# Performance work log

Hardware: AMD Instinct MI355X
Metric: run time of the kernel (lower is better)

The kernel has to match this reference:

```python
import jax, jax.numpy as jnp
import numpy as np

N_NODES = 100000
N_EDGES = 3200000
IN_DIM = 256
EMB_DIM = 64
BATCH = 4096
WEIGHT_DECAY = 1e-4


def setup_inputs() -> dict:
    key = jax.random.key(0)
    ks = jax.random.split(key, 8)
    feats = jax.random.normal(ks[0], (N_NODES, IN_DIM), dtype=jnp.float32)
    W = jax.random.normal(ks[1], (IN_DIM, EMB_DIM), dtype=jnp.float32) * (1.0 / np.sqrt(IN_DIM))
    edge_row = jax.random.randint(ks[2], (N_EDGES,), 0, N_NODES, dtype=jnp.int32)
    edge_col = jax.random.randint(ks[3], (N_EDGES,), 0, N_NODES, dtype=jnp.int32)
    edge_val = jax.random.uniform(ks[4], (N_EDGES,), dtype=jnp.float32) * 0.05  # normalized adj weights
    idx1 = jax.random.randint(ks[5], (BATCH,), 0, N_NODES, dtype=jnp.int32)
    idx2 = jax.random.randint(ks[6], (BATCH,), 0, N_NODES, dtype=jnp.int32)
    neg_idx = jax.random.randint(ks[7], (BATCH,), 0, N_NODES, dtype=jnp.int32)
    return {"feats": feats, "W": W, "edge_row": edge_row, "edge_col": edge_col,
            "edge_val": edge_val, "idx1": idx1, "idx2": idx2, "neg_idx": neg_idx}


def reference(feats, W, edge_row, edge_col, edge_val, idx1, idx2, neg_idx):
    # GraphConvolution: tanh( A_sparse @ (X @ W) ), A in COO form
    xw = feats @ W                                              # [N, D]
    msgs = edge_val[:, None] * xw[edge_col]                     # [E, D] gather + scale
    h = jax.ops.segment_sum(msgs, edge_row, num_segments=N_NODES)  # sparse-dense matmul
    h = jnp.tanh(h)
    # tf.nn.l2_normalize(embedding, 1)
    sq = jnp.sum(h * h, axis=1, keepdims=True)
    emb = h * jax.lax.rsqrt(jnp.maximum(sq, 1e-12))             # [N, D]
    # embedding lookups
    o1, o2, on = emb[idx1], emb[idx2], emb[neg_idx]             # [B, D] each
    y_ui = jnp.sum(o1 * o2, axis=1)
    y_uj = jnp.sum(o1 * on, axis=1)
    # BPR loss + weight decay (tf.nn.l2_loss = 0.5*sum(x^2))
    bpr = jnp.sum(-jax.nn.log_sigmoid(y_ui - y_uj))
    loss = (bpr + WEIGHT_DECAY * 0.5 * jnp.sum(emb * emb)) / jnp.float32(BATCH)
    return loss
```

## Files before the change

### kernel.cpp

```cpp
#include <hip/hip_runtime.h>
#include <cmath>

#define N_NODES 100000
#define N_EDGES 3200000
#define IN_DIM 256
#define EMB 64
#define BATCH 4096
#define MWAVES 6250
#define NBUCK 782
#define BROWS 128
#define BSTRIDE 4608
#define PSTRIDE 5504
#define EPB 4096

typedef unsigned long long u64;
typedef unsigned int u32;
typedef unsigned short u16;
typedef __attribute__((ext_vector_type(8))) short bf16x8;
typedef __attribute__((ext_vector_type(4))) float f32x4;

__device__ __forceinline__ float wave_sum(float v) {
#pragma unroll
    for (int m = 1; m < 64; m <<= 1) v += __shfl_xor(v, m, 64);
    return v;
}

__device__ __forceinline__ u16 f2bf_rne(float f) {
    u32 u = __float_as_uint(f);
    u32 r = ((u >> 16) & 1u) + 0x7FFFu;
    return (u16)((u + r) >> 16);
}

__device__ __forceinline__ float bf2f(u32 bits16) {
    return __uint_as_float(bits16 << 16);
}

__global__ __launch_bounds__(256) void mfma_gemm_kernel(const float* __restrict__ feats,
                                                        const float* __restrict__ W,
                                                        u16* __restrict__ xwb) {
    __shared__ u16 wlds[32 * 64 * 8];
    const int tid = threadIdx.x;
    for (int idx = tid; idx < 32 * 64; idx += 256) {
        const int f = idx >> 6, lane = idx & 63;
        const int kt = f >> 2, nt = f & 3;
        const int k0 = kt * 32 + (lane >> 4) * 8;
        const int n  = nt * 16 + (lane & 15);
        u32 buf[4];
#pragma unroll
        for (int jj = 0; jj < 4; ++jj) {
            u16 lo = f2bf_rne(W[(size_t)(k0 + 2 * jj) * EMB + n]);
            u16 hi = f2bf_rne(W[(size_t)(k0 + 2 * jj + 1) * EMB + n]);
            buf[jj] = (u32)lo | ((u32)hi << 16);
        }
        *(uint4*)&wlds[idx * 8] = *(uint4*)buf;
    }
    __syncthreads();

    const int wave = tid >> 6, lane = tid & 63;
    const int wid = blockIdx.x * 4 + wave;
    if (wid >= MWAVES) return;
    const int row0 = wid * 16;
    const int arow = row0 + (lane & 15);
    const int kbase = (lane >> 4) * 8;
    const float* fr = feats + (size_t)arow * IN_DIM + kbase;

    float4 av[16];
#pragma unroll
    for (int kt = 0; kt < 8; ++kt) {
        av[2 * kt]     = *(const float4*)(fr + kt * 32);
        av[2 * kt + 1] = *(const float4*)(fr + kt * 32 + 4);
    }

    f32x4 acc[4] = {};
    const u16* wl = &wlds[lane * 8];
#pragma unroll
    for (int kt = 0; kt < 8; ++kt) {
        float4 a0 = av[2 * kt], a1 = av[2 * kt + 1];
        u32 ab[4];
        ab[0] = (u32)f2bf_rne(a0.x) | ((u32)f2bf_rne(a0.y) << 16);
        ab[1] = (u32)f2bf_rne(a0.z) | ((u32)f2bf_rne(a0.w) << 16);
        ab[2] = (u32)f2bf_rne(a1.x) | ((u32)f2bf_rne(a1.y) << 16);
        ab[3] = (u32)f2bf_rne(a1.z) | ((u32)f2bf_rne(a1.w) << 16);
        bf16x8 afrag = *(bf16x8*)ab;
#pragma unroll
        for (int nt = 0; nt < 4; ++nt) {
            bf16x8 bfrag = *(const bf16x8*)&wl[(kt * 4 + nt) * 512];
            acc[nt] = __builtin_amdgcn_mfma_f32_16x16x32_bf16(afrag, bfrag, acc[nt], 0, 0, 0);
        }
    }
    const int rb = row0 + (lane >> 4) * 4;
    const int cb = lane & 15;
#pragma unroll
    for (int nt = 0; nt < 4; ++nt)
#pragma unroll
        for (int r = 0; r < 4; ++r)
            xwb[(size_t)(rb + r) * EMB + nt * 16 + cb] = f2bf_rne(acc[nt][r]);
}

__global__ __launch_bounds__(256) void passA_kernel(const int* __restrict__ erow,
                                                    const int* __restrict__ ecol,
                                                    const float* __restrict__ eval,
                                                    u32* __restrict__ gcursor,
                                                    u64* __restrict__ sorted) {
    __shared__ u64 stage[EPB];
    __shared__ u32 hist[1024];
    __shared__ u32 offs[1024];
    __shared__ u32 cursor[1024];
    __shared__ u32 gbase[1024];
    __shared__ u32 partial[256];

    const int tid = threadIdx.x;
    const int e0 = blockIdx.x * EPB;
    const int total = min(EPB, N_EDGES - e0);

    for (int i = tid; i < 1024; i += 256) hist[i] = 0;
    __syncthreads();

    u64 ent[16];
    int eb[16];
#pragma unroll
    for (int j = 0; j < 16; ++j) {
        const int e = e0 + j * 256 + tid;
        if (e < N_EDGES) {
            const int r = erow[e];
            const int c = ecol[e];
            const u16 vb = f2bf_rne(eval[e]);
            ent[j] = (u64)(u32)r | ((u64)(u32)c << 17) | ((u64)vb << 34);
            eb[j] = r >> 7;
            atomicAdd(&hist[eb[j]], 1u);
        } else {
            eb[j] = -1;
        }
    }
    __syncthreads();

    u32 local[4], s = 0;
#pragma unroll
    for (int q = 0; q < 4; ++q) {
        local[q] = s;
        s += hist[4 * tid + q];
    }
    partial[tid] = s;
    __syncthreads();
    for (int off = 1; off < 256; off <<= 1) {
        u32 x = (tid >= off) ? partial[tid - off] : 0;
        __syncthreads();
        partial[tid] += x;
        __syncthreads();
    }
    const u32 base = partial[tid] - s;
#pragma unroll
    for (int q = 0; q < 4; ++q) {
        offs[4 * tid + q] = base + local[q];
        cursor[4 * tid + q] = base + local[q];
    }
    __syncthreads();

#pragma unroll
    for (int j = 0; j < 16; ++j) {
        if (eb[j] >= 0) {
            u32 pos = atomicAdd(&cursor[eb[j]], 1u);
            stage[pos] = ent[j];
        }
    }
    __syncthreads();

    for (int b = tid; b < 1024; b += 256) {
        const u32 cnt = cursor[b] - offs[b];
        gbase[b] = cnt ? atomicAdd(&gcursor[b], cnt) : 0;
    }
    __syncthreads();

    for (int i = tid; i < total; i += 256) {
        const u64 p = stage[i];
        const int b = (int)(p & 0x1FFFFu) >> 7;
        const u32 gpos = gbase[b] + ((u32)i - offs[b]);
        if (gpos < BSTRIDE) sorted[(size_t)b * BSTRIDE + gpos] = p;
    }
}

__global__ __launch_bounds__(512, 6) void gather_kernel(const u16* __restrict__ xwb,
                                                        u64* __restrict__ sorted,
                                                        const u32* __restrict__ gcursor,
                                                        float* __restrict__ accumA) {
    __shared__ u64 stage[PSTRIDE];
    __shared__ u32 rhist[BROWS], roff[BROWS], rcur[BROWS], sc[BROWS];
    __shared__ float part[8];
    const int tid = threadIdx.x, wave = tid >> 6, lane = tid & 63;
    const int b = blockIdx.x;
    u64* gbase = sorted + (size_t)b * BSTRIDE;
    const int cnt = min((int)gcursor[b], BSTRIDE);

    if (tid < BROWS) rhist[tid] = 0;
    __syncthreads();

    u64 ent[9];
    int nloc = 0;
    for (int i = tid; i < cnt; i += 512) {
        u64 p = gbase[i];
        ent[nloc++] = p;
        atomicAdd(&rhist[(int)(p & 127u)], 1u);
    }
    __syncthreads();

    if (tid < BROWS) sc[tid] = (rhist[tid] + 7u) & ~7u;
    __syncthreads();
    for (int off = 1; off < BROWS; off <<= 1) {
        u32 x = (tid < BROWS && tid >= off) ? sc[tid - off] : 0;
        __syncthreads();
        if (tid < BROWS) sc[tid] += x;
        __syncthreads();
    }
    if (tid < BROWS) {
        const u32 r0 = sc[tid] - ((rhist[tid] + 7u) & ~7u);
        roff[tid] = r0;
        rcur[tid] = r0;
    }
    __syncthreads();

    for (int j = 0; j < nloc; ++j) {
        const u64 p = ent[j];
        const u32 pos = atomicAdd(&rcur[(int)(p & 127u)], 1u);
        const u32 coff = (((u32)(p >> 17)) & 0x1FFFFu) << 7;
        const u32 v32  = (((u32)(p >> 34)) & 0xFFFFu) << 16;
        stage[pos] = (u64)coff | ((u64)v32 << 32);
    }
    __syncthreads();

    if (tid < BROWS) {
        const int e = roff[tid] + rhist[tid];
        const int pe = roff[tid] + (int)((rhist[tid] + 7u) & ~7u);
        for (int k = e; k < pe; ++k) stage[k] = 0ull;
    }
    __syncthreads();

    u16* embp = (u16*)gbase;
    const int lhalf = lane >> 5;
    const int loff = (lane & 31) * 4;
    const char* xwc = (const char*)xwb;
    float wd = 0.f;
    for (int rr = 0; rr < 16; ++rr) {
        const int r = wave * 16 + rr;
        const int n8 = (int)((rhist[r] + 7u) & ~7u);
        float acc0 = 0.f, acc1 = 0.f;
        const u64* sp = &stage[roff[r] + lhalf];
        for (int j = 0; j < n8; j += 8, sp += 8) {
            u64 cv0 = sp[0], cv1 = sp[2], cv2 = sp[4], cv3 = sp[6];
            u32 x0 = *(const u32*)(xwc + ((u32)cv0 + loff));
            u32 x1 = *(const u32*)(xwc + ((u32)cv1 + loff));
            u32 x2 = *(const u32*)(xwc + ((u32)cv2 + loff));
            u32 x3 = *(const u32*)(xwc + ((u32)cv3 + loff));
            float v0 = __uint_as_float((u32)(cv0 >> 32));
            float v1 = __uint_as_float((u32)(cv1 >> 32));
            float v2 = __uint_as_float((u32)(cv2 >> 32));
            float v3 = __uint_as_float((u32)(cv3 >> 32));
            acc0 += v0 * __uint_as_float(x0 << 16);
            acc1 += v0 * __uint_as_float(x0 & 0xFFFF0000u);
            acc0 += v1 * __uint_as_float(x1 << 16);
            acc1 += v1 * __uint_as_float(x1 & 0xFFFF0000u);
            acc0 += v2 * __uint_as_float(x2 << 16);
            acc1 += v2 * __uint_as_float(x2 & 0xFFFF0000u);
            acc0 += v3 * __uint_as_float(x3 << 16);
            acc1 += v3 * __uint_as_float(x3 & 0xFFFF0000u);
        }
        acc0 += __shfl_xor(acc0, 32, 64);
        acc1 += __shfl_xor(acc1, 32, 64);
        const float t0 = tanhf(acc0);
        const float t1 = tanhf(acc1);
        float sq = t0 * t0 + t1 * t1;
#pragma unroll
        for (int m = 1; m < 32; m <<= 1) sq += __shfl_xor(sq, m, 64);
        const float rn = rsqrtf(fmaxf(sq, 1e-12f));
        if (lhalf == 0 && b * BROWS + r < N_NODES) {
            const u32 o = (u32)f2bf_rne(t0 * rn) | ((u32)f2bf_rne(t1 * rn) << 16);
            *(u32*)&embp[r * EMB + (lane & 31) * 2] = o;
        }
        wd += sq / fmaxf(sq, 1e-12f);
    }
    if (lane == 0) part[wave] = wd;
    __syncthreads();
    if (tid == 0) {
        float v = 0.f;
#pragma unroll
        for (int w = 0; w < 8; ++w) v += part[w];
        unsafeAtomicAdd(&accumA[b & 255], v);
    }
}

__device__ __forceinline__ float emb_ld(const u64* __restrict__ sorted, int row, int lane) {
    const u16* rp = (const u16*)(sorted + (size_t)(row >> 7) * BSTRIDE) + (row & 127) * EMB;
    return bf2f(rp[lane]);
}

__global__ __launch_bounds__(256) void bpr_kernel(const u64* __restrict__ sorted,
                                                  const int* __restrict__ idx1,
                                                  const int* __restrict__ idx2,
                                                  const int* __restrict__ nidx,
                                                  float* __restrict__ accumB) {
    const int wave = threadIdx.x >> 6, lane = threadIdx.x & 63;
    const int i = blockIdx.x * 4 + wave;
    float o1 = emb_ld(sorted, idx1[i], lane);
    float o2 = emb_ld(sorted, idx2[i], lane);
    float on = emb_ld(sorted, nidx[i], lane);
    float yui = wave_sum(o1 * o2);
    float yuj = wave_sum(o1 * on);
    if (lane == 0) {
        float x = yui - yuj;
        float li = (x > 0.f) ? log1pf(expf(-x)) : (-x + log1pf(expf(x)));
        unsafeAtomicAdd(&accumB[i & 255], li);
    }
}

__global__ __launch_bounds__(64) void finalize_kernel(const float* __restrict__ accumA,
                                                      const float* __restrict__ accumB,
                                                      float* __restrict__ out) {
    const int t = threadIdx.x;
    float wd = 0.f, bp = 0.f;
#pragma unroll
    for (int k = 0; k < 4; ++k) {
        wd += accumA[t + 64 * k];
        bp += accumB[t + 64 * k];
    }
    wd = wave_sum(wd);
    bp = wave_sum(bp);
    if (t == 0) out[0] = (bp + 1e-4f * 0.5f * wd) / (float)BATCH;
}

extern "C" void kernel_launch(void* const* d_in, const int* in_sizes, int n_in,
                              void* d_out, int out_size, void* d_ws, size_t ws_size,
                              hipStream_t stream) {
    const float* feats = (const float*)d_in[0];
    const float* W     = (const float*)d_in[1];
    const int*   erow  = (const int*)d_in[2];
    const int*   ecol  = (const int*)d_in[3];
    const float* eval  = (const float*)d_in[4];
    const int*   idx1  = (const int*)d_in[5];
    const int*   idx2  = (const int*)d_in[6];
    const int*   nidx  = (const int*)d_in[7];
    float* out = (float*)d_out;

    u16*   xwb     = (u16*)d_ws;
    u64*   sorted  = (u64*)(xwb + (size_t)N_NODES * EMB);
    u32*   gcursor = (u32*)(sorted + (size_t)NBUCK * BSTRIDE);
    float* accumA  = (float*)(gcursor + 1024);
    float* accumB  = accumA + 256;

    hipMemsetAsync(gcursor, 0, (1024 + 512) * sizeof(u32), stream);

    mfma_gemm_kernel<<<(MWAVES + 3) / 4, 256, 0, stream>>>(feats, W, xwb);
    passA_kernel<<<(N_EDGES + EPB - 1) / EPB, 256, 0, stream>>>(erow, ecol, eval, gcursor, sorted);
    gather_kernel<<<NBUCK, 512, 0, stream>>>(xwb, sorted, gcursor, accumA);
    bpr_kernel<<<BATCH / 4, 256, 0, stream>>>(sorted, idx1, idx2, nidx, accumB);
    finalize_kernel<<<1, 64, 0, stream>>>(accumA, accumB, out);
}
```

Before: 345.9 us.

## Gather 16-byte row slices per lane with 8 edges per wave step

```diff
diff --git a/kernel.cpp b/kernel.cpp
--- a/kernel.cpp
+++ b/kernel.cpp
@@ -179,11 +179,12 @@
     }
 }
 
-__global__ __launch_bounds__(512, 6) void gather_kernel(const u16* __restrict__ xwb,
+__global__ __launch_bounds__(512, 4) void gather_kernel(const u16* __restrict__ xwb,
                                                         u64* __restrict__ sorted,
                                                         const u32* __restrict__ gcursor,
                                                         float* __restrict__ accumA) {
-    __shared__ u64 stage[PSTRIDE];
+    __shared__ u32 scoff[PSTRIDE];
+    __shared__ u16 sval[PSTRIDE];
     __shared__ u32 rhist[BROWS], roff[BROWS], rcur[BROWS], sc[BROWS];
     __shared__ float part[8];
     const int tid = threadIdx.x, wave = tid >> 6, lane = tid & 63;
@@ -221,62 +222,88 @@
     for (int j = 0; j < nloc; ++j) {
         const u64 p = ent[j];
         const u32 pos = atomicAdd(&rcur[(int)(p & 127u)], 1u);
-        const u32 coff = (((u32)(p >> 17)) & 0x1FFFFu) << 7;
-        const u32 v32  = (((u32)(p >> 34)) & 0xFFFFu) << 16;
-        stage[pos] = (u64)coff | ((u64)v32 << 32);
+        scoff[pos] = (((u32)(p >> 17)) & 0x1FFFFu) << 7;
+        sval[pos]  = (u16)(p >> 34);
     }
     __syncthreads();
 
     if (tid < BROWS) {
         const int e = roff[tid] + rhist[tid];
         const int pe = roff[tid] + (int)((rhist[tid] + 7u) & ~7u);
-        for (int k = e; k < pe; ++k) stage[k] = 0ull;
+        for (int k = e; k < pe; ++k) { scoff[k] = 0u; sval[k] = 0; }
     }
     __syncthreads();
 
     u16* embp = (u16*)gbase;
-    const int lhalf = lane >> 5;
-    const int loff = (lane & 31) * 4;
+    const int g = lane >> 3;
+    const int eoff = (lane & 7) * 16;
+    const int g0 = g & 1, g1 = (g >> 1) & 1, g2 = (g >> 2) & 1;
+    const int el = (lane & 7) * 8 + 4 * g0 + 2 * g1 + g2;
     const char* xwc = (const char*)xwb;
     float wd = 0.f;
+
+#define FMA8(X, V)                                         \
+    acc[0] += (V) * __uint_as_float((X).x << 16);          \
+    acc[1] += (V) * __uint_as_float((X).x & 0xFFFF0000u);  \
+    acc[2] += (V) * __uint_as_float((X).y << 16);          \
+    acc[3] += (V) * __uint_as_float((X).y & 0xFFFF0000u);  \
+    acc[4] += (V) * __uint_as_float((X).z << 16);          \
+    acc[5] += (V) * __uint_as_float((X).z & 0xFFFF0000u);  \
+    acc[6] += (V) * __uint_as_float((X).w << 16);          \
+    acc[7] += (V) * __uint_as_float((X).w & 0xFFFF0000u);
+
     for (int rr = 0; rr < 16; ++rr) {
         const int r = wave * 16 + rr;
         const int n8 = (int)((rhist[r] + 7u) & ~7u);
-        float acc0 = 0.f, acc1 = 0.f;
-        const u64* sp = &stage[roff[r] + lhalf];
-        for (int j = 0; j < n8; j += 8, sp += 8) {
-            u64 cv0 = sp[0], cv1 = sp[2], cv2 = sp[4], cv3 = sp[6];
-            u32 x0 = *(const u32*)(xwc + ((u32)cv0 + loff));
-            u32 x1 = *(const u32*)(xwc + ((u32)cv1 + loff));
-            u32 x2 = *(const u32*)(xwc + ((u32)cv2 + loff));
-            u32 x3 = *(const u32*)(xwc + ((u32)cv3 + loff));
-            float v0 = __uint_as_float((u32)(cv0 >> 32));
-            float v1 = __uint_as_float((u32)(cv1 >> 32));
-            float v2 = __uint_as_float((u32)(cv2 >> 32));
-            float v3 = __uint_as_float((u32)(cv3 >> 32));
-            acc0 += v0 * __uint_as_float(x0 << 16);
-            acc1 += v0 * __uint_as_float(x0 & 0xFFFF0000u);
-            acc0 += v1 * __uint_as_float(x1 << 16);
-            acc1 += v1 * __uint_as_float(x1 & 0xFFFF0000u);
-            acc0 += v2 * __uint_as_float(x2 << 16);
-            acc1 += v2 * __uint_as_float(x2 & 0xFFFF0000u);
-            acc0 += v3 * __uint_as_float(x3 << 16);
-            acc1 += v3 * __uint_as_float(x3 & 0xFFFF0000u);
-        }
-        acc0 += __shfl_xor(acc0, 32, 64);
-        acc1 += __shfl_xor(acc1, 32, 64);
-        const float t0 = tanhf(acc0);
-        const float t1 = tanhf(acc1);
-        float sq = t0 * t0 + t1 * t1;
-#pragma unroll
-        for (int m = 1; m < 32; m <<= 1) sq += __shfl_xor(sq, m, 64);
+        const int base = (int)roff[r];
+        float acc[8] = {0.f, 0.f, 0.f, 0.f, 0.f, 0.f, 0.f, 0.f};
+
+        int j = 0;
+        for (; j + 16 <= n8; j += 16) {
+            const int i0 = base + j + g;
+            const u32 c0 = scoff[i0];
+            const u32 c1 = scoff[i0 + 8];
+            const float v0 = bf2f(sval[i0]);
+            const float v1 = bf2f(sval[i0 + 8]);
+            const uint4 x0 = *(const uint4*)(xwc + (c0 + eoff));
+            const uint4 x1 = *(const uint4*)(xwc + (c1 + eoff));
+            FMA8(x0, v0)
+            FMA8(x1, v1)
+        }
+        if (j < n8) {
+            const int i0 = base + j + g;
+            const u32 c0 = scoff[i0];
+            const float v0 = bf2f(sval[i0]);
+            const uint4 x0 = *(const uint4*)(xwc + (c0 + eoff));
+            FMA8(x0, v0)
+        }
+
+        float k4[4];
+#pragma unroll
+        for (int i = 0; i < 4; ++i) {
+            const float snd = g0 ? acc[i] : acc[i + 4];
+            const float kp  = g0 ? acc[i + 4] : acc[i];
+            k4[i] = kp + __shfl_xor(snd, 8, 64);
+        }
+        float k2[2];
+#pragma unroll
+        for (int i = 0; i < 2; ++i) {
+            const float snd = g1 ? k4[i] : k4[i + 2];
+            const float kp  = g1 ? k4[i + 2] : k4[i];
+            k2[i] = kp + __shfl_xor(snd, 16, 64);
+        }
+        const float snd = g2 ? k2[0] : k2[1];
+        const float kp  = g2 ? k2[1] : k2[0];
+        const float s = kp + __shfl_xor(snd, 32, 64);
+
+        const float t = tanhf(s);
+        const float sq = wave_sum(t * t);
         const float rn = rsqrtf(fmaxf(sq, 1e-12f));
-        if (lhalf == 0 && b * BROWS + r < N_NODES) {
-            const u32 o = (u32)f2bf_rne(t0 * rn) | ((u32)f2bf_rne(t1 * rn) << 16);
-            *(u32*)&embp[r * EMB + (lane & 31) * 2] = o;
-        }
+        if (b * BROWS + r < N_NODES)
+            embp[r * EMB + el] = f2bf_rne(t * rn);
         wd += sq / fmaxf(sq, 1e-12f);
     }
+#undef FMA8
     if (lane == 0) part[wave] = wd;
     __syncthreads();
     if (tid == 0) {
```

Result: faster. 314.4 us (-9.1%).
